# Kernel optimization log

Hardware: AMD Instinct MI355X
Metric: run time of the kernel (lower is better)

The kernel has to match this reference:

```python
import jax, jax.numpy as jnp
import numpy as np

B, T, D = 4, 2048, 1024
E = 16            # routed experts
S = 2             # shared experts
MOE_TOPK = 2
COSINE_LAMBDA = 0.1


def setup_inputs() -> dict:
    key = jax.random.key(0)
    k_x, k_g, k_sh, k_rt = jax.random.split(key, 4)
    x = jax.random.normal(k_x, (B, T, D), dtype=jnp.float32)
    gate_w = jax.random.normal(k_g, (E, D), dtype=jnp.float32) * 0.02
    gate_b = jnp.zeros((E,), dtype=jnp.float32)
    shared_experts = jax.random.normal(k_sh, (S, D), dtype=jnp.float32) * 0.1
    routed_experts = jax.random.normal(k_rt, (E, D), dtype=jnp.float32) * 0.1
    return {"x": x, "gate_w": gate_w, "gate_b": gate_b,
            "shared_experts": shared_experts, "routed_experts": routed_experts}


def reference(x, gate_w, gate_b, shared_experts, routed_experts):
    b, t, d = x.shape
    n = b * t
    hidden = x.reshape(n, d)                                   # [N, D]

    # ---- router ----
    logits = hidden @ gate_w.T + gate_b                        # [N, E]
    probs = jax.nn.softmax(logits, axis=-1)                    # stable (shift-invariant)
    topk_vals, topk_idx = jax.lax.top_k(probs, MOE_TOPK)       # [N, K]
    if MOE_TOPK == 1:
        weights = jnp.ones_like(topk_vals)
    else:
        weights = topk_vals / jnp.clip(topk_vals.sum(-1, keepdims=True), 1e-6)

    # ---- shared experts (always active): sum_e hidden * w_e ----
    shared_sum = hidden * shared_experts.sum(0)                # [N, D]

    # ---- dense all-expert elementwise scale (as in original) ----
    routed_outs = hidden[None, :, :] * routed_experts[:, None, :]   # [E, N, D]

    # ---- diversity loss: cosine sim between flattened expert outputs ----
    flat = routed_outs.reshape(E, -1)                          # [E, N*D]
    norms = jnp.maximum(jnp.linalg.norm(flat, axis=1, keepdims=True), 1e-8)
    normed = flat / norms
    sim = jnp.clip(normed @ normed.T, -1.0, 1.0)               # [E, E]
    mask = 1.0 - jnp.eye(E, dtype=sim.dtype)
    div_loss = (sim * mask).sum() / max(E * (E - 1), 1) * COSINE_LAMBDA

    # ---- top-k gather + weighted combine ----
    routed_nd = routed_outs.transpose(1, 0, 2)                 # [N, E, D]
    sel = jnp.take_along_axis(routed_nd, topk_idx[:, :, None], axis=1)  # [N, K, D]
    dyn_sum = (sel * weights[:, :, None]).sum(axis=1)          # [N, D]

    out = (shared_sum + dyn_sum).reshape(b, t, d)
    return out, div_loss
```

## Files before the change

### kernel.cpp

```cpp
#include <hip/hip_runtime.h>

#define NTOK 8192
#define DDIM 1024
#define NEXP 16
#define NPAIR 136
#define NREP 8
#define XROW 1032

#define WS_GWT 0
#define WS_SG  16384
#define WS_GP  (16384 + NREP * DDIM)

__global__ __launch_bounds__(256) void moe_prep(
    const float* __restrict__ gate_w,
    float* __restrict__ ws)
{
    const int gid = blockIdx.x * 256 + threadIdx.x;
    const int e = gid & 15;
    const int d4 = gid >> 4;
    const float4* gw4 = (const float4*)gate_w;
    float4* gwT4 = (float4*)(ws + WS_GWT);
    gwT4[d4 * 16 + e] = gw4[e * 256 + d4];
    float* s_glob = ws + WS_SG;
    s_glob[gid] = 0.f;
    s_glob[gid + 4096] = 0.f;
}

__global__ __launch_bounds__(256, 4) void moe_fused(
    const float* __restrict__ x,
    const float* __restrict__ gate_b,
    const float* __restrict__ sh,
    const float* __restrict__ re,
    float* __restrict__ out,
    float* __restrict__ ws)
{
    __shared__ float xt[8][XROW];

    const int t = threadIdx.x;
    const int b = blockIdx.x;
    const float4* gwT4 = (const float4*)(ws + WS_GWT);
    float* s_glob = ws + WS_SG;

    float4 ss = make_float4(0.f, 0.f, 0.f, 0.f);
    {
        const float4* x4 = (const float4*)x + (size_t)b * 2048;
        #pragma unroll
        for (int i = 0; i < 8; ++i) {
            float4 v = x4[i * 256 + t];
            *(float4*)&xt[i][4 * t] = v;
            ss.x = fmaf(v.x, v.x, ss.x);
            ss.y = fmaf(v.y, v.y, ss.y);
            ss.z = fmaf(v.z, v.z, ss.z);
            ss.w = fmaf(v.w, v.w, ss.w);
        }
    }
    __syncthreads();

    const int lane = t & 63;
    const int wave = t >> 6;
    const int e = lane & 15;
    const int h = (lane >> 4) & 1;
    const int g = lane >> 5;

    const int tokL = wave * 2 + g;
    const float* xrow = &xt[tokL][h * 512];
    const float4* gt = gwT4 + h * 128 * 16;
    float4 a4 = make_float4(0.f, 0.f, 0.f, 0.f);
    #pragma unroll 8
    for (int i = 0; i < 128; ++i) {
        float4 xv = *(const float4*)(xrow + 4 * i);
        float4 gv = gt[i * 16 + e];
        a4.x = fmaf(xv.x, gv.x, a4.x);
        a4.y = fmaf(xv.y, gv.y, a4.y);
        a4.z = fmaf(xv.z, gv.z, a4.z);
        a4.w = fmaf(xv.w, gv.w, a4.w);
    }
    float acc = (a4.x + a4.y) + (a4.z + a4.w);
    acc += __shfl_xor(acc, 16, 64);
    acc += gate_b[e];

    float v0 = -3.0e38f, v1 = -3.0e38f;
    int i0 = 0, i1 = 0;
    const int base = lane & 32;
    #pragma unroll
    for (int j = 0; j < NEXP; ++j) {
        float lv = __shfl(acc, base + j, 64);
        if (lv > v0)      { v1 = v0; i1 = i0; v0 = lv; i0 = j; }
        else if (lv > v1) { v1 = lv; i1 = j; }
    }
    float ex = __expf(v1 - v0);
    float w0 = 1.f / (1.f + ex);
    float w1 = ex * w0;

    float4 shs[4];
    {
        const float4* s0 = (const float4*)sh;
        const float4* s1 = (const float4*)(sh + DDIM);
        #pragma unroll
        for (int j = 0; j < 4; ++j) {
            float4 p = s0[lane + 64 * j];
            float4 q = s1[lane + 64 * j];
            shs[j] = make_float4(p.x + q.x, p.y + q.y, p.z + q.z, p.w + q.w);
        }
    }

    #pragma unroll
    for (int tk = 0; tk < 2; ++tk) {
        const int src = tk << 5;
        float a0 = __shfl(w0, src, 64);
        float a1 = __shfl(w1, src, 64);
        int   e0 = __shfl(i0, src, 64);
        int   e1 = __shfl(i1, src, 64);
        const int tokL2 = wave * 2 + tk;
        const float4* xr = (const float4*)&xt[tokL2][0];
        const float4* r0 = (const float4*)(re + (size_t)e0 * DDIM);
        const float4* r1 = (const float4*)(re + (size_t)e1 * DDIM);
        float4* o = (float4*)(out + ((size_t)b * 8 + tokL2) * DDIM);
        #pragma unroll
        for (int j = 0; j < 4; ++j) {
            float4 xv = xr[lane + 64 * j];
            float4 b0 = r0[lane + 64 * j];
            float4 b1 = r1[lane + 64 * j];
            float4 r;
            r.x = xv.x * (shs[j].x + a0 * b0.x + a1 * b1.x);
            r.y = xv.y * (shs[j].y + a0 * b0.y + a1 * b1.y);
            r.z = xv.z * (shs[j].z + a0 * b0.z + a1 * b1.z);
            r.w = xv.w * (shs[j].w + a0 * b0.w + a1 * b1.w);
            o[lane + 64 * j] = r;
        }
    }

    {
        float* rep = s_glob + (size_t)(b & (NREP - 1)) * DDIM;
        atomicAdd(&rep[4 * t + 0], ss.x);
        atomicAdd(&rep[4 * t + 1], ss.y);
        atomicAdd(&rep[4 * t + 2], ss.z);
        atomicAdd(&rep[4 * t + 3], ss.w);
    }
}

__global__ __launch_bounds__(320) void moe_div_partial(
    const float* __restrict__ re,
    const float* __restrict__ ws,
    float* __restrict__ G_part_unused)
{
    __shared__ float reT[64][17];
    __shared__ float s4[4][64];
    __shared__ float s_loc[64];

    const int t = threadIdx.x;
    const int b = blockIdx.x;
    const int d0 = b * 64;
    const float* s_glob = ws + WS_SG;
    float* G_part = (float*)(ws + WS_GP);

    if (t < 256) {
        int c = t & 63, r = t >> 6;
        s4[r][c] = s_glob[r * DDIM + d0 + c] + s_glob[(r + 4) * DDIM + d0 + c];
        int e = t >> 4, d4 = t & 15;
        float4 v = ((const float4*)(re + (size_t)e * DDIM + d0))[d4];
        reT[d4 * 4 + 0][e] = v.x;
        reT[d4 * 4 + 1][e] = v.y;
        reT[d4 * 4 + 2][e] = v.z;
        reT[d4 * 4 + 3][e] = v.w;
    }
    __syncthreads();
    if (t < 64) s_loc[t] = (s4[0][t] + s4[1][t]) + (s4[2][t] + s4[3][t]);
    __syncthreads();

    const int p = t >> 1;
    const int half = t & 1;
    float a = 0.f;
    int pe = 0, pf = 0;
    if (p < NPAIR) {
        int rem = p;
        while (rem >= NEXP - pe) { rem -= NEXP - pe; ++pe; }
        pf = pe + rem;
        #pragma unroll
        for (int i = 0; i < 32; ++i) {
            int dd = half * 32 + i;
            a += s_loc[dd] * reT[dd][pe] * reT[dd][pf];
        }
    }
    a += __shfl_down(a, 1, 64);
    if (p < NPAIR && half == 0) G_part[b * NPAIR + p] = a;
}

__global__ __launch_bounds__(192) void moe_div_final(
    const float* __restrict__ ws,
    float* __restrict__ div_out)
{
    __shared__ float G[NPAIR];
    __shared__ float nr[NEXP];
    __shared__ float lsum;
    const float* G_part = ws + WS_GP;
    const int t = threadIdx.x;

    if (t == 0) lsum = 0.f;
    if (t < NPAIR) {
        float g = 0.f;
        #pragma unroll
        for (int b = 0; b < 16; ++b) g += G_part[b * NPAIR + t];
        G[t] = g;
    }
    __syncthreads();
    if (t < NEXP) {
        int idx = t * NEXP - (t * (t - 1)) / 2;
        nr[t] = fmaxf(sqrtf(G[idx]), 1e-8f);
    }
    __syncthreads();
    if (t < NPAIR) {
        int pe = 0, rem = t;
        while (rem >= NEXP - pe) { rem -= NEXP - pe; ++pe; }
        int pf = pe + rem;
        if (pe != pf) {
            float sim = G[t] / (nr[pe] * nr[pf]);
            sim = fminf(1.f, fmaxf(-1.f, sim));
            atomicAdd(&lsum, 2.f * sim);
        }
    }
    __syncthreads();
    if (t == 0) *div_out = lsum / (float)(NEXP * (NEXP - 1)) * 0.1f;
}

extern "C" void kernel_launch(void* const* d_in, const int* in_sizes, int n_in,
                              void* d_out, int out_size, void* d_ws, size_t ws_size,
                              hipStream_t stream) {
    const float* x  = (const float*)d_in[0];
    const float* gw = (const float*)d_in[1];
    const float* gb = (const float*)d_in[2];
    const float* sh = (const float*)d_in[3];
    const float* re = (const float*)d_in[4];
    float* out = (float*)d_out;
    float* ws = (float*)d_ws;

    moe_prep<<<16, 256, 0, stream>>>(gw, ws);
    moe_fused<<<1024, 256, 0, stream>>>(x, gb, sh, re, out, ws);
    moe_div_partial<<<16, 320, 0, stream>>>(re, ws, nullptr);
    moe_div_final<<<1, 192, 0, stream>>>(ws, out + (size_t)NTOK * DDIM);
}
```

Before: 124.0 us.

## Fold diversity-loss kernels into main kernel via last-block completion counter

Removes the two separate diversity-loss kernels and instead has the last block of the fused MoE kernel (detected with an atomic counter and threadfence) reduce the per-replica sum-of-squares and compute all 136 Gram pairs and the cosine loss. This saves two kernel launches and their launch gaps. In exchange, the final reduction runs serially in one block, with 136 threads each streaming 1024 elements from global memory, and the extra per-block atomic plus fence adds a small cost to every block.

```diff
diff --git a/kernel.cpp b/kernel.cpp
--- a/kernel.cpp
+++ b/kernel.cpp
@@ -6,10 +6,11 @@
 #define NPAIR 136
 #define NREP 8
 #define XROW 1032
+#define NBLK 1024
 
 #define WS_GWT 0
 #define WS_SG  16384
-#define WS_GP  (16384 + NREP * DDIM)
+#define WS_CNT (WS_SG + NREP * DDIM)
 
 __global__ __launch_bounds__(256) void moe_prep(
     const float* __restrict__ gate_w,
@@ -24,6 +25,7 @@
     float* s_glob = ws + WS_SG;
     s_glob[gid] = 0.f;
     s_glob[gid + 4096] = 0.f;
+    if (gid == 0) ((int*)ws)[WS_CNT] = 0;
 }
 
 __global__ __launch_bounds__(256, 4) void moe_fused(
@@ -34,7 +36,10 @@
     float* __restrict__ out,
     float* __restrict__ ws)
 {
-    __shared__ float xt[8][XROW];
+    __shared__ __align__(16) float xt[8][XROW];
+    __shared__ float nr[NEXP];
+    __shared__ float lsum;
+    __shared__ int   is_last;
 
     const int t = threadIdx.x;
     const int b = blockIdx.x;
@@ -137,90 +142,61 @@
         atomicAdd(&rep[4 * t + 2], ss.z);
         atomicAdd(&rep[4 * t + 3], ss.w);
     }
-}
-
-__global__ __launch_bounds__(320) void moe_div_partial(
-    const float* __restrict__ re,
-    const float* __restrict__ ws,
-    float* __restrict__ G_part_unused)
-{
-    __shared__ float reT[64][17];
-    __shared__ float s4[4][64];
-    __shared__ float s_loc[64];
-
-    const int t = threadIdx.x;
-    const int b = blockIdx.x;
-    const int d0 = b * 64;
-    const float* s_glob = ws + WS_SG;
-    float* G_part = (float*)(ws + WS_GP);
-
-    if (t < 256) {
-        int c = t & 63, r = t >> 6;
-        s4[r][c] = s_glob[r * DDIM + d0 + c] + s_glob[(r + 4) * DDIM + d0 + c];
-        int e = t >> 4, d4 = t & 15;
-        float4 v = ((const float4*)(re + (size_t)e * DDIM + d0))[d4];
-        reT[d4 * 4 + 0][e] = v.x;
-        reT[d4 * 4 + 1][e] = v.y;
-        reT[d4 * 4 + 2][e] = v.z;
-        reT[d4 * 4 + 3][e] = v.w;
-    }
-    __syncthreads();
-    if (t < 64) s_loc[t] = (s4[0][t] + s4[1][t]) + (s4[2][t] + s4[3][t]);
-    __syncthreads();
-
-    const int p = t >> 1;
-    const int half = t & 1;
-    float a = 0.f;
+
+    __syncthreads();
+    if (t == 0) {
+        __threadfence();
+        int tk = atomicAdd((int*)ws + WS_CNT, 1);
+        is_last = (tk == NBLK - 1);
+    }
+    __syncthreads();
+    if (!is_last) return;
+    __threadfence();
+
+    float* smem = &xt[0][0];
+    {
+        const float4* sg4 = (const float4*)s_glob;
+        float4 a = sg4[t];
+        #pragma unroll
+        for (int r = 1; r < NREP; ++r) {
+            float4 v = sg4[r * 256 + t];
+            a.x += v.x; a.y += v.y; a.z += v.z; a.w += v.w;
+        }
+        ((float4*)smem)[t] = a;
+    }
+    if (t == 0) lsum = 0.f;
+    __syncthreads();
+
+    float gacc = 0.f;
     int pe = 0, pf = 0;
-    if (p < NPAIR) {
-        int rem = p;
+    if (t < NPAIR) {
+        int rem = t;
         while (rem >= NEXP - pe) { rem -= NEXP - pe; ++pe; }
         pf = pe + rem;
-        #pragma unroll
-        for (int i = 0; i < 32; ++i) {
-            int dd = half * 32 + i;
-            a += s_loc[dd] * reT[dd][pe] * reT[dd][pf];
-        }
-    }
-    a += __shfl_down(a, 1, 64);
-    if (p < NPAIR && half == 0) G_part[b * NPAIR + p] = a;
-}
-
-__global__ __launch_bounds__(192) void moe_div_final(
-    const float* __restrict__ ws,
-    float* __restrict__ div_out)
-{
-    __shared__ float G[NPAIR];
-    __shared__ float nr[NEXP];
-    __shared__ float lsum;
-    const float* G_part = ws + WS_GP;
-    const int t = threadIdx.x;
-
-    if (t == 0) lsum = 0.f;
-    if (t < NPAIR) {
-        float g = 0.f;
-        #pragma unroll
-        for (int b = 0; b < 16; ++b) g += G_part[b * NPAIR + t];
-        G[t] = g;
-    }
-    __syncthreads();
-    if (t < NEXP) {
-        int idx = t * NEXP - (t * (t - 1)) / 2;
-        nr[t] = fmaxf(sqrtf(G[idx]), 1e-8f);
-    }
-    __syncthreads();
-    if (t < NPAIR) {
-        int pe = 0, rem = t;
-        while (rem >= NEXP - pe) { rem -= NEXP - pe; ++pe; }
-        int pf = pe + rem;
-        if (pe != pf) {
-            float sim = G[t] / (nr[pe] * nr[pf]);
-            sim = fminf(1.f, fmaxf(-1.f, sim));
-            atomicAdd(&lsum, 2.f * sim);
-        }
-    }
-    __syncthreads();
-    if (t == 0) *div_out = lsum / (float)(NEXP * (NEXP - 1)) * 0.1f;
+        const float4* ra = (const float4*)(re + (size_t)pe * DDIM);
+        const float4* rb = (const float4*)(re + (size_t)pf * DDIM);
+        const float4* sl = (const float4*)smem;
+        #pragma unroll 4
+        for (int i = 0; i < 256; ++i) {
+            float4 s = sl[i];
+            float4 u = ra[i];
+            float4 v = rb[i];
+            gacc = fmaf(s.x * u.x, v.x, gacc);
+            gacc = fmaf(s.y * u.y, v.y, gacc);
+            gacc = fmaf(s.z * u.z, v.z, gacc);
+            gacc = fmaf(s.w * u.w, v.w, gacc);
+        }
+        if (pe == pf) nr[pe] = fmaxf(sqrtf(gacc), 1e-8f);
+    }
+    __syncthreads();
+    if (t < NPAIR && pe != pf) {
+        float sim = gacc / (nr[pe] * nr[pf]);
+        sim = fminf(1.f, fmaxf(-1.f, sim));
+        atomicAdd(&lsum, 2.f * sim);
+    }
+    __syncthreads();
+    if (t == 0)
+        out[(size_t)NTOK * DDIM] = lsum / (float)(NEXP * (NEXP - 1)) * 0.1f;
 }
 
 extern "C" void kernel_launch(void* const* d_in, const int* in_sizes, int n_in,
@@ -235,7 +211,5 @@
     float* ws = (float*)d_ws;
 
     moe_prep<<<16, 256, 0, stream>>>(gw, ws);
-    moe_fused<<<1024, 256, 0, stream>>>(x, gb, sh, re, out, ws);
-    moe_div_partial<<<16, 320, 0, stream>>>(re, ws, nullptr);
-    moe_div_final<<<1, 192, 0, stream>>>(ws, out + (size_t)NTOK * DDIM);
+    moe_fused<<<NBLK, 256, 0, stream>>>(x, gb, sh, re, out, ws);
 }
```

After: 174.7 us. +40.9%, slower.

## Replace atomic sum-of-squares with per-block slots and halve tokens per block

Applied to the files above, without the earlier changes.

Each fused block now handles 4 tokens instead of 8 (one token per wave, with the router dot product split four ways), and the launch grows to 2048 blocks with higher occupancy bounds. The global atomicAdd accumulation of per-dimension sums of squares is replaced by plain per-block slot writes. A new 64-block kernel reduces those slots and computes the partial Gram entries. This removes atomic contention and the zeroing pass, at the cost of an extra 8 MB of workspace writes and reads.

```diff
diff --git a/kernel.cpp b/kernel.cpp
--- a/kernel.cpp
+++ b/kernel.cpp
@@ -4,12 +4,13 @@
 #define DDIM 1024
 #define NEXP 16
 #define NPAIR 136
-#define NREP 8
 #define XROW 1032
-
-#define WS_GWT 0
-#define WS_SG  16384
-#define WS_GP  (16384 + NREP * DDIM)
+#define NBLK 2048
+#define NRED 64
+
+#define WS_GWT  0
+#define WS_SLOT 16384
+#define WS_GP   (WS_SLOT + NBLK * DDIM)
 
 __global__ __launch_bounds__(256) void moe_prep(
     const float* __restrict__ gate_w,
@@ -21,12 +22,9 @@
     const float4* gw4 = (const float4*)gate_w;
     float4* gwT4 = (float4*)(ws + WS_GWT);
     gwT4[d4 * 16 + e] = gw4[e * 256 + d4];
-    float* s_glob = ws + WS_SG;
-    s_glob[gid] = 0.f;
-    s_glob[gid + 4096] = 0.f;
-}
-
-__global__ __launch_bounds__(256, 4) void moe_fused(
+}
+
+__global__ __launch_bounds__(256, 8) void moe_fused(
     const float* __restrict__ x,
     const float* __restrict__ gate_b,
     const float* __restrict__ sh,
@@ -34,18 +32,17 @@
     float* __restrict__ out,
     float* __restrict__ ws)
 {
-    __shared__ float xt[8][XROW];
+    __shared__ __align__(16) float xt[4][XROW];
 
     const int t = threadIdx.x;
     const int b = blockIdx.x;
     const float4* gwT4 = (const float4*)(ws + WS_GWT);
-    float* s_glob = ws + WS_SG;
 
     float4 ss = make_float4(0.f, 0.f, 0.f, 0.f);
     {
-        const float4* x4 = (const float4*)x + (size_t)b * 2048;
-        #pragma unroll
-        for (int i = 0; i < 8; ++i) {
+        const float4* x4 = (const float4*)x + (size_t)b * 1024;
+        #pragma unroll
+        for (int i = 0; i < 4; ++i) {
             float4 v = x4[i * 256 + t];
             *(float4*)&xt[i][4 * t] = v;
             ss.x = fmaf(v.x, v.x, ss.x);
@@ -57,17 +54,15 @@
     __syncthreads();
 
     const int lane = t & 63;
-    const int wave = t >> 6;
+    const int wv = t >> 6;
     const int e = lane & 15;
-    const int h = (lane >> 4) & 1;
-    const int g = lane >> 5;
-
-    const int tokL = wave * 2 + g;
-    const float* xrow = &xt[tokL][h * 512];
-    const float4* gt = gwT4 + h * 128 * 16;
+    const int qr = lane >> 4;
+
+    const float* xrow = &xt[wv][qr * 256];
+    const float4* gt = gwT4 + qr * 64 * 16;
     float4 a4 = make_float4(0.f, 0.f, 0.f, 0.f);
     #pragma unroll 8
-    for (int i = 0; i < 128; ++i) {
+    for (int i = 0; i < 64; ++i) {
         float4 xv = *(const float4*)(xrow + 4 * i);
         float4 gv = gt[i * 16 + e];
         a4.x = fmaf(xv.x, gv.x, a4.x);
@@ -77,11 +72,12 @@
     }
     float acc = (a4.x + a4.y) + (a4.z + a4.w);
     acc += __shfl_xor(acc, 16, 64);
+    acc += __shfl_xor(acc, 32, 64);
     acc += gate_b[e];
 
     float v0 = -3.0e38f, v1 = -3.0e38f;
     int i0 = 0, i1 = 0;
-    const int base = lane & 32;
+    const int base = lane & 48;
     #pragma unroll
     for (int j = 0; j < NEXP; ++j) {
         float lv = __shfl(acc, base + j, 64);
@@ -99,108 +95,104 @@
         #pragma unroll
         for (int j = 0; j < 4; ++j) {
             float4 p = s0[lane + 64 * j];
-            float4 q = s1[lane + 64 * j];
-            shs[j] = make_float4(p.x + q.x, p.y + q.y, p.z + q.z, p.w + q.w);
-        }
-    }
-
-    #pragma unroll
-    for (int tk = 0; tk < 2; ++tk) {
-        const int src = tk << 5;
-        float a0 = __shfl(w0, src, 64);
-        float a1 = __shfl(w1, src, 64);
-        int   e0 = __shfl(i0, src, 64);
-        int   e1 = __shfl(i1, src, 64);
-        const int tokL2 = wave * 2 + tk;
-        const float4* xr = (const float4*)&xt[tokL2][0];
-        const float4* r0 = (const float4*)(re + (size_t)e0 * DDIM);
-        const float4* r1 = (const float4*)(re + (size_t)e1 * DDIM);
-        float4* o = (float4*)(out + ((size_t)b * 8 + tokL2) * DDIM);
+            float4 s = s1[lane + 64 * j];
+            shs[j] = make_float4(p.x + s.x, p.y + s.y, p.z + s.z, p.w + s.w);
+        }
+    }
+
+    {
+        const float4* xr = (const float4*)&xt[wv][0];
+        const float4* r0 = (const float4*)(re + (size_t)i0 * DDIM);
+        const float4* r1 = (const float4*)(re + (size_t)i1 * DDIM);
+        float4* o = (float4*)(out + ((size_t)b * 4 + wv) * DDIM);
         #pragma unroll
         for (int j = 0; j < 4; ++j) {
-            float4 xv = xr[lane + 64 * j];
-            float4 b0 = r0[lane + 64 * j];
-            float4 b1 = r1[lane + 64 * j];
+            const int idx = lane + 64 * j;
+            float4 xv = xr[idx];
+            float4 b0 = r0[idx];
+            float4 b1 = r1[idx];
             float4 r;
-            r.x = xv.x * (shs[j].x + a0 * b0.x + a1 * b1.x);
-            r.y = xv.y * (shs[j].y + a0 * b0.y + a1 * b1.y);
-            r.z = xv.z * (shs[j].z + a0 * b0.z + a1 * b1.z);
-            r.w = xv.w * (shs[j].w + a0 * b0.w + a1 * b1.w);
-            o[lane + 64 * j] = r;
-        }
-    }
-
-    {
-        float* rep = s_glob + (size_t)(b & (NREP - 1)) * DDIM;
-        atomicAdd(&rep[4 * t + 0], ss.x);
-        atomicAdd(&rep[4 * t + 1], ss.y);
-        atomicAdd(&rep[4 * t + 2], ss.z);
-        atomicAdd(&rep[4 * t + 3], ss.w);
-    }
-}
-
-__global__ __launch_bounds__(320) void moe_div_partial(
+            r.x = xv.x * (shs[j].x + w0 * b0.x + w1 * b1.x);
+            r.y = xv.y * (shs[j].y + w0 * b0.y + w1 * b1.y);
+            r.z = xv.z * (shs[j].z + w0 * b0.z + w1 * b1.z);
+            r.w = xv.w * (shs[j].w + w0 * b0.w + w1 * b1.w);
+            o[idx] = r;
+        }
+    }
+
+    *(float4*)(ws + WS_SLOT + (size_t)b * DDIM + 4 * t) = ss;
+}
+
+__global__ __launch_bounds__(256) void moe_xred_gram(
     const float* __restrict__ re,
-    const float* __restrict__ ws,
-    float* __restrict__ G_part_unused)
-{
-    __shared__ float reT[64][17];
-    __shared__ float s4[4][64];
-    __shared__ float s_loc[64];
+    float* __restrict__ ws)
+{
+    __shared__ float4 s4[64][4];
+    __shared__ float s_loc[16];
+    __shared__ float reT[16][16];
 
     const int t = threadIdx.x;
-    const int b = blockIdx.x;
-    const int d0 = b * 64;
-    const float* s_glob = ws + WS_SG;
-    float* G_part = (float*)(ws + WS_GP);
-
-    if (t < 256) {
-        int c = t & 63, r = t >> 6;
-        s4[r][c] = s_glob[r * DDIM + d0 + c] + s_glob[(r + 4) * DDIM + d0 + c];
-        int e = t >> 4, d4 = t & 15;
-        float4 v = ((const float4*)(re + (size_t)e * DDIM + d0))[d4];
-        reT[d4 * 4 + 0][e] = v.x;
-        reT[d4 * 4 + 1][e] = v.y;
-        reT[d4 * 4 + 2][e] = v.z;
-        reT[d4 * 4 + 3][e] = v.w;
-    }
-    __syncthreads();
-    if (t < 64) s_loc[t] = (s4[0][t] + s4[1][t]) + (s4[2][t] + s4[3][t]);
-    __syncthreads();
-
-    const int p = t >> 1;
-    const int half = t & 1;
-    float a = 0.f;
-    int pe = 0, pf = 0;
-    if (p < NPAIR) {
-        int rem = p;
+    const int j = blockIdx.x;
+    const int c = t & 3;
+    const int r = t >> 2;
+
+    {
+        const float4* sl4 = (const float4*)(ws + WS_SLOT);
+        const size_t colbase = (size_t)4 * j + c;
+        float4 acc = make_float4(0.f, 0.f, 0.f, 0.f);
+        #pragma unroll 8
+        for (int k = 0; k < 32; ++k) {
+            float4 v = sl4[(size_t)(r + 64 * k) * 256 + colbase];
+            acc.x += v.x; acc.y += v.y; acc.z += v.z; acc.w += v.w;
+        }
+        s4[r][c] = acc;
+    }
+    {
+        const int e = t >> 4, dd = t & 15;
+        reT[dd][e] = re[(size_t)e * DDIM + 16 * j + dd];
+    }
+    __syncthreads();
+
+    if (t < 4) {
+        float4 a = s4[0][t];
+        for (int rr = 1; rr < 64; ++rr) {
+            float4 v = s4[rr][t];
+            a.x += v.x; a.y += v.y; a.z += v.z; a.w += v.w;
+        }
+        s_loc[4 * t + 0] = a.x;
+        s_loc[4 * t + 1] = a.y;
+        s_loc[4 * t + 2] = a.z;
+        s_loc[4 * t + 3] = a.w;
+    }
+    __syncthreads();
+
+    if (t < NPAIR) {
+        int pe = 0, rem = t;
         while (rem >= NEXP - pe) { rem -= NEXP - pe; ++pe; }
-        pf = pe + rem;
-        #pragma unroll
-        for (int i = 0; i < 32; ++i) {
-            int dd = half * 32 + i;
+        const int pf = pe + rem;
+        float a = 0.f;
+        #pragma unroll
+        for (int dd = 0; dd < 16; ++dd)
             a += s_loc[dd] * reT[dd][pe] * reT[dd][pf];
-        }
-    }
-    a += __shfl_down(a, 1, 64);
-    if (p < NPAIR && half == 0) G_part[b * NPAIR + p] = a;
-}
-
-__global__ __launch_bounds__(192) void moe_div_final(
+        (ws + WS_GP)[j * NPAIR + t] = a;
+    }
+}
+
+__global__ __launch_bounds__(192) void moe_final(
     const float* __restrict__ ws,
     float* __restrict__ div_out)
 {
     __shared__ float G[NPAIR];
     __shared__ float nr[NEXP];
     __shared__ float lsum;
-    const float* G_part = ws + WS_GP;
     const int t = threadIdx.x;
 
     if (t == 0) lsum = 0.f;
     if (t < NPAIR) {
+        const float* gp = ws + WS_GP;
         float g = 0.f;
-        #pragma unroll
-        for (int b = 0; b < 16; ++b) g += G_part[b * NPAIR + t];
+        #pragma unroll 8
+        for (int jj = 0; jj < NRED; ++jj) g += gp[jj * NPAIR + t];
         G[t] = g;
     }
     __syncthreads();
@@ -212,7 +204,7 @@
     if (t < NPAIR) {
         int pe = 0, rem = t;
         while (rem >= NEXP - pe) { rem -= NEXP - pe; ++pe; }
-        int pf = pe + rem;
+        const int pf = pe + rem;
         if (pe != pf) {
             float sim = G[t] / (nr[pe] * nr[pf]);
             sim = fminf(1.f, fmaxf(-1.f, sim));
@@ -235,7 +227,7 @@
     float* ws = (float*)d_ws;
 
     moe_prep<<<16, 256, 0, stream>>>(gw, ws);
-    moe_fused<<<1024, 256, 0, stream>>>(x, gb, sh, re, out, ws);
-    moe_div_partial<<<16, 320, 0, stream>>>(re, ws, nullptr);
-    moe_div_final<<<1, 192, 0, stream>>>(ws, out + (size_t)NTOK * DDIM);
-}
+    moe_fused<<<NBLK, 256, 0, stream>>>(x, gb, sh, re, out, ws);
+    moe_xred_gram<<<NRED, 256, 0, stream>>>(re, ws);
+    moe_final<<<1, 192, 0, stream>>>(ws, out + (size_t)NTOK * DDIM);
+}
```

Measured after the change: 130.0 us. 4.8% more time.
